# Kernel optimization log

Measured on AMD Instinct MI355X. Metric: run time of the kernel, lower is better.

Reference implementation:

```python
import jax, jax.numpy as jnp
import numpy as np

N_QUBITS = 12
N_LAYERS = 4
BATCH = 4096
OUT_DIM = 12


def _ry(theta):
    theta = jnp.asarray(theta, jnp.float32)
    c, s = jnp.cos(theta / 2), jnp.sin(theta / 2)
    U = jnp.stack([jnp.stack([c, -s], -1), jnp.stack([s, c], -1)], -2)
    return U.astype(jnp.complex64)


def _rx(theta):
    theta = jnp.asarray(theta, jnp.float32)
    c = jnp.cos(theta / 2).astype(jnp.complex64)
    s = (-1j) * jnp.sin(theta / 2).astype(jnp.complex64)
    return jnp.stack([jnp.stack([c, s], -1), jnp.stack([s, c], -1)], -2)


def _rz(theta):
    theta = jnp.asarray(theta, jnp.float32)
    e = jnp.exp((-0.5j) * theta.astype(jnp.complex64))
    z = jnp.zeros_like(e)
    return jnp.stack([jnp.stack([e, z], -1), jnp.stack([z, jnp.conj(e)], -1)], -2)


def _apply_1q(psi, U, w):
    # psi: (B,) + (2,)*n; U: (2,2) shared gate or (B,2,2) per-sample gate
    psi = jnp.moveaxis(psi, w + 1, 1)
    if U.ndim == 2:
        psi = jnp.einsum('ij,bj...->bi...', U, psi)
    else:
        psi = jnp.einsum('bij,bj...->bi...', U, psi)
    return jnp.moveaxis(psi, 1, w + 1)


def _cnot(psi, c, t):
    # flip target axis where control bit == 1
    psi = jnp.moveaxis(psi, (c + 1, t + 1), (1, 2))
    psi = psi.at[:, 1].set(psi[:, 1, ::-1])
    return jnp.moveaxis(psi, (1, 2), (c + 1, t + 1))


def _pauli_z_signs(n):
    idx = np.arange(2 ** n)
    bits = (idx[None, :] >> (n - 1 - np.arange(n))[:, None]) & 1  # wire 0 = MSB
    return jnp.asarray(1.0 - 2.0 * bits, jnp.float32)  # (n, 2^n)


def _quantum_forward(x, quantum_weights):
    b, n = x.shape[0], N_QUBITS
    # tf.nn.l2_normalize(sample, axis=0) per sample
    xn = x * jax.lax.rsqrt(jnp.maximum(jnp.sum(x * x, axis=1, keepdims=True), 1e-12))
    # angle encoding: pi * x / (max|x| + 1e-8)
    angles = jnp.pi * xn / (jnp.max(jnp.abs(xn), axis=1, keepdims=True) + 1e-8)
    psi = jnp.zeros((b, 2 ** n), jnp.complex64).at[:, 0].set(1.0)
    psi = psi.reshape((b,) + (2,) * n)
    # data encoding: RY(angles[i]) on wire i (per-sample batched gates)
    for i in range(n):
        psi = _apply_1q(psi, _ry(angles[:, i]), i)
    # variational layers: RX/RY/RZ per qubit, then CNOT ring
    for layer in range(N_LAYERS):
        base = layer * 3 * n
        for i in range(n):
            p = base + 3 * i
            psi = _apply_1q(psi, _rx(quantum_weights[p]), i)
            psi = _apply_1q(psi, _ry(quantum_weights[p + 1]), i)
            psi = _apply_1q(psi, _rz(quantum_weights[p + 2]), i)
        for i in range(n):
            psi = _cnot(psi, i, (i + 1) % n)
    psi = psi.reshape(b, -1)
    probs = jnp.real(psi) ** 2 + jnp.imag(psi) ** 2  # (B, 2^n)
    return probs @ _pauli_z_signs(n).T  # (B, n): <Z_i> per qubit


def setup_inputs() -> dict:
    key = jax.random.key(0)
    k1, k2, k3 = jax.random.split(key, 3)
    n_params = 3 * N_QUBITS * N_LAYERS
    return {
        'x': jax.random.normal(k1, (BATCH, N_QUBITS), jnp.float32),
        'quantum_weights': jax.random.uniform(k2, (n_params,), jnp.float32, -0.05, 0.05),
        'dense_w': jax.random.normal(k3, (N_QUBITS, OUT_DIM), jnp.float32) / np.sqrt(N_QUBITS),
        'dense_b': jnp.zeros((OUT_DIM,), jnp.float32),
    }


def reference(x, quantum_weights, dense_w, dense_b):
    q = _quantum_forward(x, quantum_weights)
    return jnp.tanh(q @ dense_w + dense_b)
```

## Files before the change

kernel.cpp:

```cpp
#include <hip/hip_runtime.h>
#include <math.h>

#define NQ   12
#define NL   4
#define BLK  256

typedef float v4f  __attribute__((ext_vector_type(4)));
typedef __fp16 v8h __attribute__((ext_vector_type(8)));

__device__ __forceinline__ constexpr int sigma_inv_c(int i) {
    int j = i;
    for (int c = 0; c < NQ; ++c) {
        int t = (c + 1) % NQ;
        int cb = (j >> (NQ - 1 - c)) & 1;
        j ^= cb << (NQ - 1 - t);
    }
    return j;
}

__device__ __forceinline__ constexpr int lswz(int l) {
    return l ^ (((l >> 3) ^ (l >> 7)) & 7);
}

__device__ __forceinline__ unsigned pk2(float a, float b) {
    return __builtin_bit_cast(unsigned, __builtin_amdgcn_cvt_pkrtz(a, b));
}

__device__ __forceinline__ int fslot(int k, int n) {
    return ((k >> 3) * 16 + n) * 8 + (k & 7);
}

__global__ __launch_bounds__(BLK) void gate_kernel(
    const float* __restrict__ qw, __fp16* __restrict__ gout)
{
    __shared__ float G[NL * NQ][8];
    const int t = threadIdx.x;
    if (t < NL * NQ) {
        const int p = (t / NQ) * 3 * NQ + 3 * (t % NQ);
        float t1 = qw[p], t2 = qw[p + 1], t3 = qw[p + 2];
        float a, b, c, d, gr, h;
        sincosf(0.5f * t1, &b, &a);
        sincosf(0.5f * t2, &d, &c);
        sincosf(0.5f * t3, &h, &gr);
        float m00r =  c * a, m00i =  d * b;
        float m01r = -d * a, m01i = -c * b;
        float m10r =  d * a, m10i = -c * b;
        float m11r =  c * a, m11i = -d * b;
        float* g = G[t];
        g[0] = gr * m00r + h * m00i;  g[1] = gr * m00i - h * m00r;
        g[2] = gr * m01r + h * m01i;  g[3] = gr * m01i - h * m01r;
        g[4] = gr * m10r - h * m10i;  g[5] = gr * m10i + h * m10r;
        g[6] = gr * m11r - h * m11i;  g[7] = gr * m11i + h * m11r;
    }
    __syncthreads();
    const int n = t & 15, r = t >> 4;
    for (int mat = 0; mat < 12; ++mat) {
        const int layer = mat / 3, ph = mat % 3;
        const int wbase = (ph == 0) ? 8 : (ph == 1) ? 4 : 0;
        float cr = 1.f, ci = 0.f;
        #pragma unroll
        for (int b = 0; b < 4; ++b) {
            const float* g = G[layer * NQ + wbase + b];
            const int rb = (r >> (3 - b)) & 1, nb = (n >> (3 - b)) & 1;
            const float er = g[(nb * 2 + rb) * 2], ei = g[(nb * 2 + rb) * 2 + 1];
            const float xr = cr * er - ci * ei, xi = cr * ei + ci * er;
            cr = xr; ci = xi;
        }
        __fp16* b1 = gout + (mat * 2 + 0) * 512;
        __fp16* b2 = gout + (mat * 2 + 1) * 512;
        b1[fslot(2 * r, n)]     = (__fp16)cr;
        b1[fslot(2 * r + 1, n)] = (__fp16)(-ci);
        b2[fslot(2 * r, n)]     = (__fp16)ci;
        b2[fslot(2 * r + 1, n)] = (__fp16)cr;
    }
}

#define READ_FRAGS(SRC)                                                     \
    _Pragma("unroll")                                                       \
    for (int q = 0; q < 4; ++q)                                             \
        af[q] = __builtin_bit_cast(v8h, *(const uint4*)&sh[(SRC) +          \
                    lswz((((wv) << 6) | (q << 4) | nn) * 4 + g) * 8]);

#define MFMA_PHASE(MAT)                                                     \
    { const v8h b1 = gf[((MAT) * 2 + 0) * 64 + lane];                       \
      const v8h b2 = gf[((MAT) * 2 + 1) * 64 + lane];                       \
      _Pragma("unroll")                                                     \
      for (int q = 0; q < 4; ++q) {                                         \
          d1[q] = __builtin_amdgcn_mfma_f32_16x16x32_f16(af[q], b1, zf, 0, 0, 0); \
          d2[q] = __builtin_amdgcn_mfma_f32_16x16x32_f16(af[q], b2, zf, 0, 0, 0); \
      } }

#define WRITE_COLS(DST)                                                     \
    _Pragma("unroll")                                                       \
    for (int q = 0; q < 4; ++q) {                                           \
        const int CCn = (nn << 4) | (wv << 2) | q;                          \
        *(uint4*)&sh[(DST) + lswz(CCn * 4 + g) * 8] =                       \
            make_uint4(pk2(d1[q].x, d2[q].x), pk2(d1[q].y, d2[q].y),        \
                       pk2(d1[q].z, d2[q].z), pk2(d1[q].w, d2[q].w));       \
    }

#define WRITE_SIGMA(DST)                                                    \
    _Pragma("unroll")                                                       \
    for (int q = 0; q < 4; ++q) {                                           \
        const int iq = ifix ^ sigma_inv_c(q << 4);                          \
        _Pragma("unroll")                                                   \
        for (int rg = 0; rg < 4; ++rg) {                                    \
            const int ii = iq ^ sigma_inv_c(rg);                            \
            *(unsigned*)&sh[(DST) + lswz(ii >> 2) * 8 + (ii & 3) * 2] =     \
                pk2(d1[q][rg], d2[q][rg]);                                  \
        }                                                                   \
    }

__global__ __launch_bounds__(BLK) void qsim_kernel(
    const float* __restrict__ x,
    const __fp16* __restrict__ gates,
    const float* __restrict__ dw,
    const float* __restrict__ db,
    float* __restrict__ out)
{
    __shared__ __align__(16) __fp16 sh[16384];
    float* xv    = (float*)sh;
    float* enc_c = (float*)sh + 16;
    float* enc_s = (float*)sh + 32;
    float* red   = (float*)sh;

    const int tid  = threadIdx.x;
    const int lane = tid & 63;
    const int wv   = tid >> 6;
    const int s    = blockIdx.x;
    const int nn = lane & 15, g = lane >> 4;
    const v8h* gf = (const v8h*)gates;
    const v4f zf = {0.f, 0.f, 0.f, 0.f};

    if (tid < NQ) xv[tid] = x[s * NQ + tid];
    __syncthreads();
    if (tid < NQ) {
        float ss = 0.f;
        #pragma unroll
        for (int j = 0; j < NQ; ++j) ss += xv[j] * xv[j];
        float inv = rsqrtf(fmaxf(ss, 1e-12f));
        float mx = 0.f;
        #pragma unroll
        for (int j = 0; j < NQ; ++j) mx = fmaxf(mx, fabsf(xv[j] * inv));
        float ang = 3.14159265358979323846f * (xv[tid] * inv) / (mx + 1e-8f);
        float cc, sn;
        sincosf(0.5f * ang, &sn, &cc);
        enc_c[tid] = cc; enc_s[tid] = sn;
    }
    __syncthreads();

    v8h af[4];
    {
        #define PICK(W, B) ((B) ? enc_s[W] : enc_c[W])
        float R4[4];
        #pragma unroll
        for (int t = 0; t < 4; ++t) {
            const int r = 4 * g + t;
            R4[t] = PICK(8, (r >> 3) & 1) * PICK(9, (r >> 2) & 1)
                  * PICK(10, (r >> 1) & 1) * PICK(11, r & 1);
        }
        const float Pfix = PICK(0, (wv >> 1) & 1) * PICK(1, wv & 1)
                         * PICK(4, (nn >> 3) & 1) * PICK(5, (nn >> 2) & 1)
                         * PICK(6, (nn >> 1) & 1) * PICK(7, nn & 1);
        #pragma unroll
        for (int q = 0; q < 4; ++q) {
            const float Pq = Pfix * PICK(2, (q >> 1) & 1) * PICK(3, q & 1);
            #pragma unroll
            for (int t = 0; t < 4; ++t) {
                af[q][2 * t]     = (__fp16)(Pq * R4[t]);
                af[q][2 * t + 1] = (__fp16)0.f;
            }
        }
        #undef PICK
    }
    __syncthreads();

    const int ifix = sigma_inv_c((nn << 8) | (wv << 6) | (g << 2));

    v4f d1[4], d2[4];
    #pragma unroll 1
    for (int l = 0; l < NL; ++l) {
        const int XA = (l & 1) * 8192;
        const int XB = 8192 - XA;

        if (l > 0) { READ_FRAGS(XB) }
        MFMA_PHASE(l * 3 + 0)
        WRITE_COLS(XA)
        __syncthreads();

        READ_FRAGS(XA)
        MFMA_PHASE(l * 3 + 1)
        WRITE_COLS(XB)
        __syncthreads();

        READ_FRAGS(XB)
        MFMA_PHASE(l * 3 + 2)
        if (l < NL - 1) {
            WRITE_SIGMA(XA)
            __syncthreads();
        }
    }

    float pr[16];
    #pragma unroll
    for (int q = 0; q < 4; ++q)
        #pragma unroll
        for (int rg = 0; rg < 4; ++rg)
            pr[q * 4 + rg] = d1[q][rg] * d1[q][rg] + d2[q][rg] * d2[q][rg];
    #pragma unroll
    for (int st = 1; st < 16; st <<= 1) {
        #pragma unroll
        for (int i = 0; i < 16; ++i) {
            if (!(i & st)) {
                const float a = pr[i], b = pr[i ^ st];
                pr[i] = a + b; pr[i ^ st] = a - b;
            }
        }
    }
    float vals[NQ];
    #pragma unroll
    for (int w = 0; w < NQ; ++w) {
        const int sb = 11 - w;
        const int f = (((sigma_inv_c(0x20) >> sb) & 1) << 3)
                    | (((sigma_inv_c(0x10) >> sb) & 1) << 2)
                    | (((sigma_inv_c(2)    >> sb) & 1) << 1)
                    |  ((sigma_inv_c(1)    >> sb) & 1);
        const float v = pr[f];
        vals[w] = ((ifix >> sb) & 1) ? -v : v;
    }
    #pragma unroll
    for (int m = 1; m <= 32; m <<= 1) {
        #pragma unroll
        for (int w = 0; w < NQ; ++w) vals[w] += __shfl_xor(vals[w], m);
    }
    __syncthreads();
    if (lane == 0) {
        #pragma unroll
        for (int w = 0; w < NQ; ++w) red[wv * NQ + w] = vals[w];
    }
    __syncthreads();
    if (tid < NQ)
        red[48 + tid] = red[tid] + red[NQ + tid] + red[2 * NQ + tid] + red[3 * NQ + tid];
    __syncthreads();
    if (tid < NQ) {
        float v = db[tid];
        #pragma unroll
        for (int w = 0; w < NQ; ++w) v += red[48 + w] * dw[w * NQ + tid];
        out[s * NQ + tid] = tanhf(v);
    }
}

extern "C" void kernel_launch(void* const* d_in, const int* in_sizes, int n_in,
                              void* d_out, int out_size, void* d_ws, size_t ws_size,
                              hipStream_t stream) {
    const float* x  = (const float*)d_in[0];
    const float* qw = (const float*)d_in[1];
    const float* dw = (const float*)d_in[2];
    const float* db = (const float*)d_in[3];
    float* out = (float*)d_out;
    __fp16* gates = (__fp16*)d_ws;
    int batch = in_sizes[0] / NQ;
    gate_kernel<<<1, BLK, 0, stream>>>(qw, gates);
    qsim_kernel<<<batch, BLK, 0, stream>>>(x, gates, dw, db, out);
}
```

Measured before the change: 121.4 us.

## Single-buffer LDS state to raise occupancy and parallelize gate kernel over blocks

The simulation kernel drops its ping-pong LDS double buffer, halving shared memory to 16KB per block, and adds barriers between reading fragments and overwriting the same buffer. A min-blocks-per-CU launch bound of 8 is also added. The gate precompute kernel now runs 12 blocks, one per gate matrix, instead of looping serially in a single block. The aim is more resident blocks per CU and a shorter prologue kernel, paid for with extra barriers per layer and possible register pressure from the launch bound.

```diff
diff --git a/kernel.cpp b/kernel.cpp
--- a/kernel.cpp
+++ b/kernel.cpp
@@ -33,10 +33,12 @@
 __global__ __launch_bounds__(BLK) void gate_kernel(
     const float* __restrict__ qw, __fp16* __restrict__ gout)
 {
-    __shared__ float G[NL * NQ][8];
+    __shared__ float G[NQ][8];
     const int t = threadIdx.x;
-    if (t < NL * NQ) {
-        const int p = (t / NQ) * 3 * NQ + 3 * (t % NQ);
+    const int mat = blockIdx.x;
+    const int layer = mat / 3, ph = mat - 3 * layer;
+    if (t < NQ) {
+        const int p = layer * 3 * NQ + 3 * t;
         float t1 = qw[p], t2 = qw[p + 1], t3 = qw[p + 2];
         float a, b, c, d, gr, h;
         sincosf(0.5f * t1, &b, &a);
@@ -54,25 +56,22 @@
     }
     __syncthreads();
     const int n = t & 15, r = t >> 4;
-    for (int mat = 0; mat < 12; ++mat) {
-        const int layer = mat / 3, ph = mat % 3;
-        const int wbase = (ph == 0) ? 8 : (ph == 1) ? 4 : 0;
-        float cr = 1.f, ci = 0.f;
-        #pragma unroll
-        for (int b = 0; b < 4; ++b) {
-            const float* g = G[layer * NQ + wbase + b];
-            const int rb = (r >> (3 - b)) & 1, nb = (n >> (3 - b)) & 1;
-            const float er = g[(nb * 2 + rb) * 2], ei = g[(nb * 2 + rb) * 2 + 1];
-            const float xr = cr * er - ci * ei, xi = cr * ei + ci * er;
-            cr = xr; ci = xi;
-        }
-        __fp16* b1 = gout + (mat * 2 + 0) * 512;
-        __fp16* b2 = gout + (mat * 2 + 1) * 512;
-        b1[fslot(2 * r, n)]     = (__fp16)cr;
-        b1[fslot(2 * r + 1, n)] = (__fp16)(-ci);
-        b2[fslot(2 * r, n)]     = (__fp16)ci;
-        b2[fslot(2 * r + 1, n)] = (__fp16)cr;
-    }
+    const int wbase = (ph == 0) ? 8 : (ph == 1) ? 4 : 0;
+    float cr = 1.f, ci = 0.f;
+    #pragma unroll
+    for (int b = 0; b < 4; ++b) {
+        const float* g = G[wbase + b];
+        const int rb = (r >> (3 - b)) & 1, nb = (n >> (3 - b)) & 1;
+        const float er = g[(nb * 2 + rb) * 2], ei = g[(nb * 2 + rb) * 2 + 1];
+        const float xr = cr * er - ci * ei, xi = cr * ei + ci * er;
+        cr = xr; ci = xi;
+    }
+    __fp16* b1 = gout + (mat * 2 + 0) * 512;
+    __fp16* b2 = gout + (mat * 2 + 1) * 512;
+    b1[fslot(2 * r, n)]     = (__fp16)cr;
+    b1[fslot(2 * r + 1, n)] = (__fp16)(-ci);
+    b2[fslot(2 * r, n)]     = (__fp16)ci;
+    b2[fslot(2 * r + 1, n)] = (__fp16)cr;
 }
 
 #define READ_FRAGS(SRC)                                                     \
@@ -111,14 +110,14 @@
         }                                                                   \
     }
 
-__global__ __launch_bounds__(BLK) void qsim_kernel(
+__global__ __launch_bounds__(BLK, 8) void qsim_kernel(
     const float* __restrict__ x,
     const __fp16* __restrict__ gates,
     const float* __restrict__ dw,
     const float* __restrict__ db,
     float* __restrict__ out)
 {
-    __shared__ __align__(16) __fp16 sh[16384];
+    __shared__ __align__(16) __fp16 sh[8192];
     float* xv    = (float*)sh;
     float* enc_c = (float*)sh + 16;
     float* enc_s = (float*)sh + 32;
@@ -180,23 +179,25 @@
     v4f d1[4], d2[4];
     #pragma unroll 1
     for (int l = 0; l < NL; ++l) {
-        const int XA = (l & 1) * 8192;
-        const int XB = 8192 - XA;
-
-        if (l > 0) { READ_FRAGS(XB) }
+        if (l > 0) {
+            READ_FRAGS(0)
+            __syncthreads();
+        }
         MFMA_PHASE(l * 3 + 0)
-        WRITE_COLS(XA)
-        __syncthreads();
-
-        READ_FRAGS(XA)
+        WRITE_COLS(0)
+        __syncthreads();
+
+        READ_FRAGS(0)
+        __syncthreads();
         MFMA_PHASE(l * 3 + 1)
-        WRITE_COLS(XB)
-        __syncthreads();
-
-        READ_FRAGS(XB)
+        WRITE_COLS(0)
+        __syncthreads();
+
+        READ_FRAGS(0)
+        __syncthreads();
         MFMA_PHASE(l * 3 + 2)
         if (l < NL - 1) {
-            WRITE_SIGMA(XA)
+            WRITE_SIGMA(0)
             __syncthreads();
         }
     }
@@ -260,6 +261,6 @@
     float* out = (float*)d_out;
     __fp16* gates = (__fp16*)d_ws;
     int batch = in_sizes[0] / NQ;
-    gate_kernel<<<1, BLK, 0, stream>>>(qw, gates);
+    gate_kernel<<<12, BLK, 0, stream>>>(qw, gates);
     qsim_kernel<<<batch, BLK, 0, stream>>>(x, gates, dw, db, out);
 }
```

Result: slower. 140.8 us (+15.9%).

## Derive second gate fragment in registers, interleave MFMA with stores, parallelize gate kernel

Applied to the files above, without the earlier changes.

The second B fragment (imaginary-part companion) is now rebuilt from the first by a half-word swap and a sign flip, instead of being loaded from global memory. This halves gate fragment loads per phase. MFMA results are written to shared memory per q iteration instead of after all MFMAs, which lowers live accumulator registers and lets stores overlap matrix ops. The gate precompute kernel is split across 12 blocks, one per matrix, instead of looping serially in a single block.

```diff
diff --git a/kernel.cpp b/kernel.cpp
--- a/kernel.cpp
+++ b/kernel.cpp
@@ -7,6 +7,7 @@
 
 typedef float v4f  __attribute__((ext_vector_type(4)));
 typedef __fp16 v8h __attribute__((ext_vector_type(8)));
+typedef unsigned v4u __attribute__((ext_vector_type(4)));
 
 __device__ __forceinline__ constexpr int sigma_inv_c(int i) {
     int j = i;
@@ -26,6 +27,17 @@
     return __builtin_bit_cast(unsigned, __builtin_amdgcn_cvt_pkrtz(a, b));
 }
 
+__device__ __forceinline__ v8h derive_b2(v8h b1) {
+    v4u w = __builtin_bit_cast(v4u, b1);
+    v4u r;
+    #pragma unroll
+    for (int i = 0; i < 4; ++i) {
+        const unsigned rot = (w[i] >> 16) | (w[i] << 16);
+        r[i] = rot ^ 0x8000u;
+    }
+    return __builtin_bit_cast(v8h, r);
+}
+
 __device__ __forceinline__ int fslot(int k, int n) {
     return ((k >> 3) * 16 + n) * 8 + (k & 7);
 }
@@ -33,10 +45,12 @@
 __global__ __launch_bounds__(BLK) void gate_kernel(
     const float* __restrict__ qw, __fp16* __restrict__ gout)
 {
-    __shared__ float G[NL * NQ][8];
+    __shared__ float G[NQ][8];
     const int t = threadIdx.x;
-    if (t < NL * NQ) {
-        const int p = (t / NQ) * 3 * NQ + 3 * (t % NQ);
+    const int mat = blockIdx.x;
+    const int layer = mat / 3, ph = mat - 3 * layer;
+    if (t < NQ) {
+        const int p = layer * 3 * NQ + 3 * t;
         float t1 = qw[p], t2 = qw[p + 1], t3 = qw[p + 2];
         float a, b, c, d, gr, h;
         sincosf(0.5f * t1, &b, &a);
@@ -54,25 +68,22 @@
     }
     __syncthreads();
     const int n = t & 15, r = t >> 4;
-    for (int mat = 0; mat < 12; ++mat) {
-        const int layer = mat / 3, ph = mat % 3;
-        const int wbase = (ph == 0) ? 8 : (ph == 1) ? 4 : 0;
-        float cr = 1.f, ci = 0.f;
-        #pragma unroll
-        for (int b = 0; b < 4; ++b) {
-            const float* g = G[layer * NQ + wbase + b];
-            const int rb = (r >> (3 - b)) & 1, nb = (n >> (3 - b)) & 1;
-            const float er = g[(nb * 2 + rb) * 2], ei = g[(nb * 2 + rb) * 2 + 1];
-            const float xr = cr * er - ci * ei, xi = cr * ei + ci * er;
-            cr = xr; ci = xi;
-        }
-        __fp16* b1 = gout + (mat * 2 + 0) * 512;
-        __fp16* b2 = gout + (mat * 2 + 1) * 512;
-        b1[fslot(2 * r, n)]     = (__fp16)cr;
-        b1[fslot(2 * r + 1, n)] = (__fp16)(-ci);
-        b2[fslot(2 * r, n)]     = (__fp16)ci;
-        b2[fslot(2 * r + 1, n)] = (__fp16)cr;
-    }
+    const int wbase = (ph == 0) ? 8 : (ph == 1) ? 4 : 0;
+    float cr = 1.f, ci = 0.f;
+    #pragma unroll
+    for (int b = 0; b < 4; ++b) {
+        const float* g = G[wbase + b];
+        const int rb = (r >> (3 - b)) & 1, nb = (n >> (3 - b)) & 1;
+        const float er = g[(nb * 2 + rb) * 2], ei = g[(nb * 2 + rb) * 2 + 1];
+        const float xr = cr * er - ci * ei, xi = cr * ei + ci * er;
+        cr = xr; ci = xi;
+    }
+    __fp16* b1 = gout + (mat * 2 + 0) * 512;
+    __fp16* b2 = gout + (mat * 2 + 1) * 512;
+    b1[fslot(2 * r, n)]     = (__fp16)cr;
+    b1[fslot(2 * r + 1, n)] = (__fp16)(-ci);
+    b2[fslot(2 * r, n)]     = (__fp16)ci;
+    b2[fslot(2 * r + 1, n)] = (__fp16)cr;
 }
 
 #define READ_FRAGS(SRC)                                                     \
@@ -81,35 +92,42 @@
         af[q] = __builtin_bit_cast(v8h, *(const uint4*)&sh[(SRC) +          \
                     lswz((((wv) << 6) | (q << 4) | nn) * 4 + g) * 8]);
 
+#define MW_COLS(MAT, DST)                                                   \
+    { const v8h b1 = gf[((MAT) * 2 + 0) * 64 + lane];                       \
+      const v8h b2 = derive_b2(b1);                                         \
+      _Pragma("unroll")                                                     \
+      for (int q = 0; q < 4; ++q) {                                         \
+          const v4f e1 = __builtin_amdgcn_mfma_f32_16x16x32_f16(af[q], b1, zf, 0, 0, 0); \
+          const v4f e2 = __builtin_amdgcn_mfma_f32_16x16x32_f16(af[q], b2, zf, 0, 0, 0); \
+          const int CCn = (nn << 4) | (wv << 2) | q;                        \
+          *(uint4*)&sh[(DST) + lswz(CCn * 4 + g) * 8] =                     \
+              make_uint4(pk2(e1.x, e2.x), pk2(e1.y, e2.y),                  \
+                         pk2(e1.z, e2.z), pk2(e1.w, e2.w));                 \
+      } }
+
+#define MW_SIGMA(MAT, DST)                                                  \
+    { const v8h b1 = gf[((MAT) * 2 + 0) * 64 + lane];                       \
+      const v8h b2 = derive_b2(b1);                                         \
+      _Pragma("unroll")                                                     \
+      for (int q = 0; q < 4; ++q) {                                         \
+          const v4f e1 = __builtin_amdgcn_mfma_f32_16x16x32_f16(af[q], b1, zf, 0, 0, 0); \
+          const v4f e2 = __builtin_amdgcn_mfma_f32_16x16x32_f16(af[q], b2, zf, 0, 0, 0); \
+          const int iq = ifix ^ sigma_inv_c(q << 4);                        \
+          _Pragma("unroll")                                                 \
+          for (int rg = 0; rg < 4; ++rg) {                                  \
+              const int ii = iq ^ sigma_inv_c(rg);                          \
+              *(unsigned*)&sh[(DST) + lswz(ii >> 2) * 8 + (ii & 3) * 2] =   \
+                  pk2(e1[rg], e2[rg]);                                      \
+          } } }
+
 #define MFMA_PHASE(MAT)                                                     \
     { const v8h b1 = gf[((MAT) * 2 + 0) * 64 + lane];                       \
-      const v8h b2 = gf[((MAT) * 2 + 1) * 64 + lane];                       \
+      const v8h b2 = derive_b2(b1);                                         \
       _Pragma("unroll")                                                     \
       for (int q = 0; q < 4; ++q) {                                         \
           d1[q] = __builtin_amdgcn_mfma_f32_16x16x32_f16(af[q], b1, zf, 0, 0, 0); \
           d2[q] = __builtin_amdgcn_mfma_f32_16x16x32_f16(af[q], b2, zf, 0, 0, 0); \
       } }
-
-#define WRITE_COLS(DST)                                                     \
-    _Pragma("unroll")                                                       \
-    for (int q = 0; q < 4; ++q) {                                           \
-        const int CCn = (nn << 4) | (wv << 2) | q;                          \
-        *(uint4*)&sh[(DST) + lswz(CCn * 4 + g) * 8] =                       \
-            make_uint4(pk2(d1[q].x, d2[q].x), pk2(d1[q].y, d2[q].y),        \
-                       pk2(d1[q].z, d2[q].z), pk2(d1[q].w, d2[q].w));       \
-    }
-
-#define WRITE_SIGMA(DST)                                                    \
-    _Pragma("unroll")                                                       \
-    for (int q = 0; q < 4; ++q) {                                           \
-        const int iq = ifix ^ sigma_inv_c(q << 4);                          \
-        _Pragma("unroll")                                                   \
-        for (int rg = 0; rg < 4; ++rg) {                                    \
-            const int ii = iq ^ sigma_inv_c(rg);                            \
-            *(unsigned*)&sh[(DST) + lswz(ii >> 2) * 8 + (ii & 3) * 2] =     \
-                pk2(d1[q][rg], d2[q][rg]);                                  \
-        }                                                                   \
-    }
 
 __global__ __launch_bounds__(BLK) void qsim_kernel(
     const float* __restrict__ x,
@@ -184,20 +202,19 @@
         const int XB = 8192 - XA;
 
         if (l > 0) { READ_FRAGS(XB) }
-        MFMA_PHASE(l * 3 + 0)
-        WRITE_COLS(XA)
+        MW_COLS(l * 3 + 0, XA)
         __syncthreads();
 
         READ_FRAGS(XA)
-        MFMA_PHASE(l * 3 + 1)
-        WRITE_COLS(XB)
+        MW_COLS(l * 3 + 1, XB)
         __syncthreads();
 
         READ_FRAGS(XB)
-        MFMA_PHASE(l * 3 + 2)
         if (l < NL - 1) {
-            WRITE_SIGMA(XA)
+            MW_SIGMA(l * 3 + 2, XA)
             __syncthreads();
+        } else {
+            MFMA_PHASE(l * 3 + 2)
         }
     }
 
@@ -260,6 +277,6 @@
     float* out = (float*)d_out;
     __fp16* gates = (__fp16*)d_ws;
     int batch = in_sizes[0] / NQ;
-    gate_kernel<<<1, BLK, 0, stream>>>(qw, gates);
+    gate_kernel<<<12, BLK, 0, stream>>>(qw, gates);
     qsim_kernel<<<batch, BLK, 0, stream>>>(x, gates, dw, db, out);
 }
```

Measured after the change: 138.4 us. +13.9%, slower.
